# Kernel optimization log

Measured on AMD Instinct MI355X. Metric: run time of the kernel, lower is better.

The kernel has to match this reference:

```python
import jax, jax.numpy as jnp
import numpy as np

IN_F = 4096
OUT_F = 4096
RANK = 8
ALPHA = 8
SCALE = ALPHA / RANK


def setup_inputs() -> dict:
    key = jax.random.key(0)
    kx, kw, kb, ka = jax.random.split(key, 4)
    x = jax.random.normal(kx, (4, 4096, IN_F), dtype=jnp.float32)
    # base frozen linear params (torch Linear default init style, any values ok)
    W = jax.random.normal(kw, (OUT_F, IN_F), dtype=jnp.float32) * (1.0 / np.sqrt(IN_F))
    b = jax.random.normal(kb, (OUT_F,), dtype=jnp.float32) * 0.01
    # lora_A: kaiming_uniform_(a=sqrt(5)) -> U(-bound, bound), bound = sqrt(6/((1+5)*in_f)) = 1/sqrt(in_f)
    bound = 1.0 / np.sqrt(IN_F)
    lora_A = jax.random.uniform(ka, (RANK, IN_F), dtype=jnp.float32, minval=-bound, maxval=bound)
    # lora_B initialized to zeros per module; use small random values so the LoRA path is exercised
    lora_B = jax.random.normal(jax.random.fold_in(key, 7), (OUT_F, RANK), dtype=jnp.float32) * 0.02
    return {"x": x, "W": W, "b": b, "lora_A": lora_A, "lora_B": lora_B}


def reference(x, W, b, lora_A, lora_B):
    # base: x @ W.T + b  [B,S,out_f]
    base = jnp.einsum("bsi,oi->bso", x, W) + b
    # low-rank path: (x @ A.T) @ B.T * scale
    xa = jnp.einsum("bsi,ri->bsr", x, lora_A)  # [B,S,r]
    lora = jnp.einsum("bsr,or->bso", xa, lora_B)
    return base + lora * SCALE
```

## Files before the change

### kernel.cpp

```cpp
#include <hip/hip_runtime.h>
#include <cstdint>

#define K_IN   4096
#define N_OUT  4096
#define M_ROWS 16384
#define RANK   8
#define LSCALE 1.0f
#define NT     64
#define ROWB   8192
#define AHALF  1048576

typedef __attribute__((ext_vector_type(8))) short  short8;
typedef __attribute__((ext_vector_type(4))) float  floatx4;

__device__ __forceinline__ unsigned short f2bf(float f) {
  uint32_t u = __float_as_uint(f);
  u += 0x7FFFu + ((u >> 16) & 1u);
  return (unsigned short)(u >> 16);
}

__global__ __launch_bounds__(256) void fold_w_kernel(
    const float* __restrict__ W, const float* __restrict__ lA,
    const float* __restrict__ lB, unsigned short* __restrict__ Weff) {
  int idx = blockIdx.x * 256 + threadIdx.x;
  int o = idx >> 10;
  int k = (idx & 1023) << 2;
  float4 w = *reinterpret_cast<const float4*>(W + (size_t)o * K_IN + k);
#pragma unroll
  for (int r = 0; r < RANK; ++r) {
    float s = LSCALE * lB[o * RANK + r];
    float4 a = *reinterpret_cast<const float4*>(lA + r * K_IN + k);
    w.x += s * a.x; w.y += s * a.y; w.z += s * a.z; w.w += s * a.w;
  }
  ushort4 p;
  p.x = f2bf(w.x); p.y = f2bf(w.y); p.z = f2bf(w.z); p.w = f2bf(w.w);
  *reinterpret_cast<ushort4*>(Weff + (size_t)o * K_IN + k) = p;
}

__global__ __launch_bounds__(256) void cvt_x_kernel(
    const float* __restrict__ x, unsigned short* __restrict__ xb) {
  size_t i = ((size_t)blockIdx.x * 256 + threadIdx.x) * 8;
  float4 a = *reinterpret_cast<const float4*>(x + i);
  float4 c = *reinterpret_cast<const float4*>(x + i + 4);
  uint4 v;
  v.x = (uint32_t)f2bf(a.x) | ((uint32_t)f2bf(a.y) << 16);
  v.y = (uint32_t)f2bf(a.z) | ((uint32_t)f2bf(a.w) << 16);
  v.z = (uint32_t)f2bf(c.x) | ((uint32_t)f2bf(c.y) << 16);
  v.w = (uint32_t)f2bf(c.z) | ((uint32_t)f2bf(c.w) << 16);
  *reinterpret_cast<uint4*>(xb + i) = v;
}

__device__ __forceinline__ void gload_lds16(const void* g, void* l) {
  __builtin_amdgcn_global_load_lds(
      (const __attribute__((address_space(1))) void*)g,
      (__attribute__((address_space(3))) void*)l, 16, 0, 0);
}

#define BAR() do { asm volatile("" ::: "memory");                         \
    __builtin_amdgcn_s_barrier();                                         \
    asm volatile("" ::: "memory"); } while (0)

#define DSR(DST, ADDR, IMM)                                               \
  asm volatile("ds_read_b128 %0, %1 offset:%2"                            \
               : "=v"(DST) : "v"(ADDR), "i"(IMM))
#define LGKM(N) do {                                                      \
    asm volatile("s_waitcnt lgkmcnt(" #N ")" ::: "memory");               \
    __builtin_amdgcn_sched_barrier(0); } while (0)

__global__ __launch_bounds__(512, 2) void gemm256_kernel(
    const unsigned short* __restrict__ Xb, const unsigned short* __restrict__ Wb,
    const float* __restrict__ bias, float* __restrict__ out) {
  __shared__ alignas(16) char lds[2 * 65536];

  const int tid  = threadIdx.x;
  const int wave = tid >> 6, lane = tid & 63;
  const int wr = wave >> 2, wc = wave & 3;
  const int l15 = lane & 15, sq = lane >> 4;

  int bx  = blockIdx.x;
  int sbx = (bx & 7) * 128 + (bx >> 3);
  const int mt = sbx >> 4;
  const int nt = sbx & 15;

  const int rstg = tid >> 3;
  const int cbst = (((tid & 7) ^ ((tid >> 3) & 7)) << 4);
  const char* aBase = (const char*)Xb + (size_t)(mt * 256 + rstg) * ROWB + cbst;
  const char* bBase = (const char*)Wb + (size_t)(nt * 256 + rstg) * ROWB + cbst;

#define STAGE_TH(TH, HH) do {                                             \
    const char* src_ = ((HH) < 2 ? aBase + (size_t)(HH) * AHALF           \
                                 : bBase + (size_t)((HH) - 2) * AHALF)    \
                       + (TH) * 128;                                      \
    char* dst_ = lds + ((TH) & 1) * 65536 + (HH) * 16384 + tid * 16;      \
    gload_lds16(src_, dst_);                                              \
    gload_lds16(src_ + (size_t)64 * ROWB, dst_ + 8192);                   \
  } while (0)
#define STAGE_TILE(TH) do {                                               \
    STAGE_TH(TH, 0); STAGE_TH(TH, 1); STAGE_TH(TH, 2); STAGE_TH(TH, 3);   \
  } while (0)

  const unsigned ldsb = (unsigned)(unsigned long long)
      (__attribute__((address_space(3))) char*)lds;
  const unsigned X = (unsigned)((l15 & 7) << 4);
  const unsigned aRow = ldsb + wr * 16384 + l15 * 128;
  const unsigned bRow = ldsb + (2 + (wc >> 1)) * 16384 + (wc & 1) * 8192
                        + l15 * 128;
  unsigned aCur0 = aRow + ((0u  + sq * 16) ^ X);
  unsigned aCur1 = aRow + ((64u + sq * 16) ^ X);
  unsigned bCur0 = bRow + ((0u  + sq * 16) ^ X);
  unsigned bCur1 = bRow + ((64u + sq * 16) ^ X);

#define LOAD_B4(DST, NQ) do {                                             \
    DSR(DST[0], bCur0, (NQ) * 4096);                                      \
    DSR(DST[1], bCur0, (NQ) * 4096 + 2048);                               \
    DSR(DST[2], bCur1, (NQ) * 4096);                                      \
    DSR(DST[3], bCur1, (NQ) * 4096 + 2048);                               \
  } while (0)
#define MFMA_Q(MQ, NQ, AF, BF) do {                                       \
    __builtin_amdgcn_s_setprio(1);                                        \
    _Pragma("unroll")                                                     \
    for (int ks = 0; ks < 2; ++ks)                                        \
      _Pragma("unroll")                                                   \
      for (int fi = 0; fi < 4; ++fi)                                      \
        _Pragma("unroll")                                                 \
        for (int fj = 0; fj < 2; ++fj)                                    \
          acc[(MQ) * 4 + fi][(NQ) * 2 + fj] =                             \
              __builtin_amdgcn_mfma_f32_16x16x32_bf16(                    \
                  AF[ks * 4 + fi], BF[ks * 2 + fj],                       \
                  acc[(MQ) * 4 + fi][(NQ) * 2 + fj], 0, 0, 0);            \
    __builtin_amdgcn_s_setprio(0); } while (0)

  floatx4 acc[8][4];
#pragma unroll
  for (int i = 0; i < 8; ++i)
#pragma unroll
    for (int j = 0; j < 4; ++j)
      acc[i][j] = (floatx4){0.f, 0.f, 0.f, 0.f};

  STAGE_TILE(0);
  STAGE_TILE(1);
  asm volatile("s_waitcnt vmcnt(8)" ::: "memory");
  BAR();

  short8 afA[8], afB[8], bfC[4], bfD[4];
#pragma unroll
  for (int fi = 0; fi < 4; ++fi) DSR(afA[fi],     aCur0, fi * 2048);
#pragma unroll
  for (int fi = 0; fi < 4; ++fi) DSR(afA[4 + fi], aCur1, fi * 2048);
  LOAD_B4(bfC, 0);

  for (int t = 0; t < NT; ++t) {
    LOAD_B4(bfD, 1);
    DSR(afB[0], aCur0, 8192);
    DSR(afB[1], aCur0, 8192 + 2048);
    LGKM(6);
    MFMA_Q(0, 0, afA, bfC);
    BAR();

    DSR(afB[2], aCur0, 8192 + 2 * 2048);
    DSR(afB[3], aCur0, 8192 + 3 * 2048);
    DSR(afB[4], aCur1, 8192);
    DSR(afB[5], aCur1, 8192 + 2048);
    DSR(afB[6], aCur1, 8192 + 2 * 2048);
    DSR(afB[7], aCur1, 8192 + 3 * 2048);
    LGKM(8);
    MFMA_Q(0, 1, afA, bfD);
    asm volatile("s_waitcnt vmcnt(0)" ::: "memory");
    BAR();

    if (t <= NT - 2) {
      aCur0 ^= 65536u; aCur1 ^= 65536u; bCur0 ^= 65536u; bCur1 ^= 65536u;
#pragma unroll
      for (int fi = 0; fi < 4; ++fi) DSR(afA[fi], aCur0, fi * 2048);
      DSR(afA[4], aCur1, 0);
      DSR(afA[5], aCur1, 2048);
      LGKM(6);
    } else {
      LGKM(0);
    }
    MFMA_Q(1, 0, afB, bfC);
    BAR();

    if (t <= NT - 2) {
      DSR(afA[6], aCur1, 2 * 2048);
      DSR(afA[7], aCur1, 3 * 2048);
      LOAD_B4(bfC, 0);
    }
    if (t <= NT - 3) STAGE_TILE(t + 2);
    __builtin_amdgcn_sched_barrier(0);
    MFMA_Q(1, 1, afB, bfD);
    BAR();
  }
#undef STAGE_TH
#undef STAGE_TILE
#undef LOAD_B4
#undef MFMA_Q

  const int row0 = mt * 256 + wr * 128 + sq * 4;
  const int col0 = nt * 256 + wc * 64 + l15;
#pragma unroll
  for (int j = 0; j < 4; ++j) {
    int col = col0 + j * 16;
    float bv = bias[col];
#pragma unroll
    for (int i = 0; i < 8; ++i) {
      int rowb = row0 + i * 16;
#pragma unroll
      for (int rr = 0; rr < 4; ++rr)
        out[(size_t)(rowb + rr) * N_OUT + col] = acc[i][j][rr] + bv;
    }
  }
}

__global__ __launch_bounds__(256) void fallback_kernel(
    const float* __restrict__ x, const float* __restrict__ W,
    const float* __restrict__ bias, const float* __restrict__ lA,
    const float* __restrict__ lB, float* __restrict__ out) {
  __shared__ float Xs[64][17];
  __shared__ float Ws[64][17];
  int tid = threadIdx.x;
  int tx = tid & 15, ty = tid >> 4;
  int bm = blockIdx.y * 64, bn = blockIdx.x * 64;
  float acc[4][4] = {};
  for (int k0 = 0; k0 < K_IN; k0 += 16) {
#pragma unroll
    for (int q = 0; q < 4; ++q) {
      int flat = q * 256 + tid;
      int r = flat >> 4, c = flat & 15;
      Xs[r][c] = x[(size_t)(bm + r) * K_IN + k0 + c];
      float w = W[(size_t)(bn + r) * K_IN + k0 + c];
#pragma unroll
      for (int rr = 0; rr < RANK; ++rr)
        w += LSCALE * lB[(bn + r) * RANK + rr] * lA[rr * K_IN + k0 + c];
      Ws[r][c] = w;
    }
    __syncthreads();
#pragma unroll
    for (int kk = 0; kk < 16; ++kk) {
      float av[4], bv[4];
#pragma unroll
      for (int i = 0; i < 4; ++i) av[i] = Xs[ty * 4 + i][kk];
#pragma unroll
      for (int j = 0; j < 4; ++j) bv[j] = Ws[tx * 4 + j][kk];
#pragma unroll
      for (int i = 0; i < 4; ++i)
#pragma unroll
        for (int j = 0; j < 4; ++j) acc[i][j] += av[i] * bv[j];
    }
    __syncthreads();
  }
#pragma unroll
  for (int i = 0; i < 4; ++i)
#pragma unroll
    for (int j = 0; j < 4; ++j)
      out[(size_t)(bm + ty * 4 + i) * N_OUT + bn + tx * 4 + j] =
          acc[i][j] + bias[bn + tx * 4 + j];
}

extern "C" void kernel_launch(void* const* d_in, const int* in_sizes, int n_in,
                              void* d_out, int out_size, void* d_ws, size_t ws_size,
                              hipStream_t stream) {
  const float* x  = (const float*)d_in[0];
  const float* W  = (const float*)d_in[1];
  const float* b  = (const float*)d_in[2];
  const float* lA = (const float*)d_in[3];
  const float* lB = (const float*)d_in[4];
  float* out = (float*)d_out;

  const size_t weff_bytes = (size_t)N_OUT * K_IN * 2;
  const size_t xb_bytes   = (size_t)M_ROWS * K_IN * 2;

  if (ws_size >= weff_bytes + xb_bytes) {
    unsigned short* Weff = (unsigned short*)d_ws;
    unsigned short* Xb   = (unsigned short*)((char*)d_ws + weff_bytes);
    fold_w_kernel<<<(int)(((size_t)N_OUT * K_IN / 4) / 256), 256, 0, stream>>>(W, lA, lB, Weff);
    cvt_x_kernel<<<(int)(((size_t)M_ROWS * K_IN / 8) / 256), 256, 0, stream>>>(x, Xb);
    gemm256_kernel<<<(M_ROWS / 256) * (N_OUT / 256), 512, 0, stream>>>(Xb, Weff, b, out);
  } else {
    dim3 grid(N_OUT / 64, M_ROWS / 64);
    fallback_kernel<<<grid, 256, 0, stream>>>(x, W, b, lA, lB, out);
  }
}
```

Before: 649.7 us.

## Restructure GEMM main loop to two barriers per iteration with batched LDS reads

Reorganises the inner k-loop of the bf16 MFMA GEMM from four barrier-separated phases into two. A and B fragments are now read from LDS in whole batches, using a new LOAD_A macro and both B halves preloaded, instead of being interleaved piecemeal between MFMA quarters. The aim is to cut workgroup synchronisation overhead per tile. The trade-off is less fine-grained overlap between LDS reads and MFMA work, and the scheduling barrier that pinned the global staging relative to the final MFMA quarter is removed.

```diff
diff --git a/kernel.cpp b/kernel.cpp
--- a/kernel.cpp
+++ b/kernel.cpp
@@ -110,6 +110,14 @@
   unsigned bCur0 = bRow + ((0u  + sq * 16) ^ X);
   unsigned bCur1 = bRow + ((64u + sq * 16) ^ X);
 
+#define LOAD_A(DST, MQ) do {                                              \
+    _Pragma("unroll")                                                     \
+    for (int fi = 0; fi < 4; ++fi)                                        \
+      DSR(DST[fi],     aCur0, (MQ) * 8192 + fi * 2048);                   \
+    _Pragma("unroll")                                                     \
+    for (int fi = 0; fi < 4; ++fi)                                        \
+      DSR(DST[4 + fi], aCur1, (MQ) * 8192 + fi * 2048);                   \
+  } while (0)
 #define LOAD_B4(DST, NQ) do {                                             \
     DSR(DST[0], bCur0, (NQ) * 4096);                                      \
     DSR(DST[1], bCur0, (NQ) * 4096 + 2048);                               \
@@ -143,56 +151,38 @@
   BAR();
 
   short8 afA[8], afB[8], bfC[4], bfD[4];
-#pragma unroll
-  for (int fi = 0; fi < 4; ++fi) DSR(afA[fi],     aCur0, fi * 2048);
-#pragma unroll
-  for (int fi = 0; fi < 4; ++fi) DSR(afA[4 + fi], aCur1, fi * 2048);
+  LOAD_A(afA, 0);
   LOAD_B4(bfC, 0);
+  LOAD_B4(bfD, 1);
 
   for (int t = 0; t < NT; ++t) {
-    LOAD_B4(bfD, 1);
-    DSR(afB[0], aCur0, 8192);
-    DSR(afB[1], aCur0, 8192 + 2048);
-    LGKM(6);
+    LOAD_A(afB, 1);
+    LGKM(12);
     MFMA_Q(0, 0, afA, bfC);
-    BAR();
-
-    DSR(afB[2], aCur0, 8192 + 2 * 2048);
-    DSR(afB[3], aCur0, 8192 + 3 * 2048);
-    DSR(afB[4], aCur1, 8192);
-    DSR(afB[5], aCur1, 8192 + 2048);
-    DSR(afB[6], aCur1, 8192 + 2 * 2048);
-    DSR(afB[7], aCur1, 8192 + 3 * 2048);
     LGKM(8);
     MFMA_Q(0, 1, afA, bfD);
-    asm volatile("s_waitcnt vmcnt(0)" ::: "memory");
+    if (t <= NT - 2) asm volatile("s_waitcnt vmcnt(0)" ::: "memory");
     BAR();
 
     if (t <= NT - 2) {
       aCur0 ^= 65536u; aCur1 ^= 65536u; bCur0 ^= 65536u; bCur1 ^= 65536u;
-#pragma unroll
-      for (int fi = 0; fi < 4; ++fi) DSR(afA[fi], aCur0, fi * 2048);
-      DSR(afA[4], aCur1, 0);
-      DSR(afA[5], aCur1, 2048);
-      LGKM(6);
+      LOAD_A(afA, 0);
+      LGKM(8);
     } else {
       LGKM(0);
     }
     MFMA_Q(1, 0, afB, bfC);
+    MFMA_Q(1, 1, afB, bfD);
+    if (t <= NT - 2) {
+      LOAD_B4(bfC, 0);
+      LOAD_B4(bfD, 1);
+    }
     BAR();
-
-    if (t <= NT - 2) {
-      DSR(afA[6], aCur1, 2 * 2048);
-      DSR(afA[7], aCur1, 3 * 2048);
-      LOAD_B4(bfC, 0);
-    }
     if (t <= NT - 3) STAGE_TILE(t + 2);
-    __builtin_amdgcn_sched_barrier(0);
-    MFMA_Q(1, 1, afB, bfD);
-    BAR();
   }
 #undef STAGE_TH
 #undef STAGE_TILE
+#undef LOAD_A
 #undef LOAD_B4
 #undef MFMA_Q
 
```

New measurement: 714.8 us. 1.1x slower.
